# Optimization experiments

Hardware: AMD Instinct MI355X
Metric: run time of the kernel (lower is better)

Reference implementation:

```python
import jax, jax.numpy as jnp
import numpy as np

N_NODES = 100000
N_EDGES = 3200000
N_GRAPHS = 512
IN_CH = 50
HID = 256


def setup_inputs() -> dict:
    key = jax.random.key(0)
    ks = jax.random.split(key, 8)
    x = jax.random.normal(ks[0], (N_NODES, IN_CH), dtype=jnp.float32)
    edge_index = jax.random.randint(ks[1], (2, N_EDGES), 0, N_NODES, dtype=jnp.int64)
    batch = jnp.sort(jax.random.randint(ks[2], (N_NODES,), 0, N_GRAPHS, dtype=jnp.int64))
    # SAGEConv params: lin_l (applied to aggregated neighbors, with bias), lin_r (root, no bias)
    s_in = 1.0 / np.sqrt(IN_CH)
    W_l = jax.random.uniform(ks[3], (HID, IN_CH), jnp.float32, -s_in, s_in)
    b_l = jax.random.uniform(ks[4], (HID,), jnp.float32, -s_in, s_in)
    W_r = jax.random.uniform(ks[5], (HID, IN_CH), jnp.float32, -s_in, s_in)
    s_h = 1.0 / np.sqrt(HID)
    W_c = jax.random.uniform(ks[6], (2, HID), jnp.float32, -s_h, s_h)
    b_c = jax.random.uniform(ks[7], (2,), jnp.float32, -s_h, s_h)
    return {"x": x, "edge_index": edge_index, "batch": batch,
            "W_l": W_l, "b_l": b_l, "W_r": W_r, "W_c": W_c, "b_c": b_c}


def _segment_mean(vals, seg_ids, num_segments):
    s = jax.ops.segment_sum(vals, seg_ids, num_segments=num_segments)
    cnt = jax.ops.segment_sum(jnp.ones((vals.shape[0],), vals.dtype), seg_ids,
                              num_segments=num_segments)
    return s / jnp.maximum(cnt, 1.0)[:, None]


def reference(x, edge_index, batch, W_l, b_l, W_r, W_c, b_c):
    src, dst = edge_index[0], edge_index[1]
    # SAGEConv: mean-aggregate neighbor features at each target node
    agg = _segment_mean(x[src], dst, N_NODES)          # [N, IN_CH]
    h = agg @ W_l.T + b_l + x @ W_r.T                  # [N, HID]
    h = jax.nn.leaky_relu(h, negative_slope=0.01)
    # dropout p=0.3 is identity in eval mode
    pooled = _segment_mean(h, batch, N_GRAPHS)         # [G, HID]
    return pooled @ W_c.T + b_c                        # [G, 2]
```

## Files before the change

### kernel.cpp

```cpp
#include <hip/hip_runtime.h>

#define N_NODES 100000
#define N_EDGES 3200000
#define N_GRAPHS 512
#define IN_CH 50
#define HID 256
#define NB 391
#define NBLK2 391
#define EPB2 8192

typedef unsigned short ushort_t;
using s16x8 = __attribute__((ext_vector_type(8))) short;
using us8   = __attribute__((ext_vector_type(8))) unsigned short;
using us4   = __attribute__((ext_vector_type(4))) unsigned short;
using f32x4 = __attribute__((ext_vector_type(4))) float;
using f32x2 = __attribute__((ext_vector_type(2))) float;

__device__ __forceinline__ float bf2f(ushort_t u) {
    return __uint_as_float(((unsigned int)u) << 16);
}
__device__ __forceinline__ ushort_t f2bf(float f) {
    unsigned int x = __float_as_uint(f);
    unsigned int r = x + 0x7fffu + ((x >> 16) & 1u);
    return (ushort_t)(r >> 16);
}
__device__ __forceinline__ int clampi(int v, int hi) {
    return v < 0 ? 0 : (v >= hi ? hi - 1 : v);
}

__device__ __forceinline__ unsigned char f2e4(float f) {
    unsigned char s = (unsigned char)((__float_as_uint(f) >> 31) << 7);
    float a = fabsf(f);
    if (a >= 0.015625f) {
        if (a > 448.f) a = 448.f;
        unsigned int u = __float_as_uint(a);
        u += 0x7FFFFu + ((u >> 20) & 1u);
        int e8 = (int)(u >> 23) - 127 + 7;
        unsigned int m8 = (u >> 20) & 7u;
        if (e8 > 15) { e8 = 15; m8 = 6; }
        return s | (unsigned char)((e8 << 3) | m8);
    } else {
        int m = (int)rintf(a * 512.f);
        if (m > 7) return s | 0x08;
        return s | (unsigned char)m;
    }
}
__device__ __forceinline__ float e42f(unsigned int c) {
    unsigned int w = ((c & 0x80u) << 24) | ((c & 0x7fu) << 20);
    return __uint_as_float(w) * 0x1p120f;
}

#if __has_builtin(__builtin_amdgcn_cvt_pk_f32_fp8)
#define ACC4(w, m, pb)                                                     \
    do {                                                                   \
        f32x2 p01 = __builtin_amdgcn_cvt_pk_f32_fp8((int)(w), false);      \
        f32x2 p23 = __builtin_amdgcn_cvt_pk_f32_fp8((int)(w), true);       \
        a2[(pb) + 0] = p01 * (m) + a2[(pb) + 0];                           \
        a2[(pb) + 1] = p23 * (m) + a2[(pb) + 1];                           \
    } while (0)
#else
#define ACC4(w, m, pb)                                                     \
    do {                                                                   \
        f32x2 p01, p23;                                                    \
        p01[0] = e42f((w) & 0xffu);        p01[1] = e42f(((w) >> 8) & 0xffu);  \
        p23[0] = e42f(((w) >> 16) & 0xffu); p23[1] = e42f(((w) >> 24) & 0xffu); \
        a2[(pb) + 0] = p01 * (m) + a2[(pb) + 0];                           \
        a2[(pb) + 1] = p23 * (m) + a2[(pb) + 1];                           \
    } while (0)
#endif

constexpr size_t OFF_GACC   = 0;
constexpr size_t ZBYTES     = 8192;
constexpr size_t OFF_AGG    = 561536;
constexpr size_t OFF_X8     = 13361536;
constexpr size_t OFF_EP     = 19761536;
constexpr size_t OFF_WT     = 32573824;
constexpr size_t OFF_BND    = 32639360;
constexpr size_t OFF_LST    = 32641416;

__global__ __launch_bounds__(512) void k_scatter(const int* __restrict__ ei,
                                                 int* __restrict__ ep,
                                                 ushort_t* __restrict__ lst) {
    __shared__ int hist[NB];
    __shared__ int sa[512];
    __shared__ int sorig[512];
    __shared__ int lstart[NB + 1];
    __shared__ int lcur[NB];
    __shared__ unsigned int eph[EPB2];

    const int blk = blockIdx.x, t = threadIdx.x;
    for (int i = t; i < NB; i += 512) hist[i] = 0;
    __syncthreads();
    const int e0 = blk * EPB2;
    int sv[16], dv[16];
#pragma unroll
    for (int j = 0; j < 16; ++j) {
        int e = e0 + j * 512 + t;
        if (e < N_EDGES) {
            sv[j] = clampi(ei[e], N_NODES);
            dv[j] = clampi(ei[N_EDGES + e], N_NODES);
        } else {
            dv[j] = -1;
        }
    }
#pragma unroll
    for (int j = 0; j < 16; ++j)
        if (dv[j] >= 0) atomicAdd(&hist[dv[j] >> 8], 1);
    __syncthreads();
    int v = (t < NB) ? hist[t] : 0;
    sa[t] = v; sorig[t] = v;
    __syncthreads();
    for (int off = 1; off < 512; off <<= 1) {
        int u = (t >= off) ? sa[t - off] : 0;
        __syncthreads();
        sa[t] += u;
        __syncthreads();
    }
    if (t < NB) { lstart[t] = sa[t] - sorig[t]; lcur[t] = sa[t] - sorig[t]; }
    if (t == NB - 1) lstart[NB] = sa[t];
    __syncthreads();
#pragma unroll
    for (int j = 0; j < 16; ++j) {
        if (dv[j] >= 0) {
            int b = dv[j] >> 8;
            int r = atomicAdd(&lcur[b], 1);
            eph[r] = ((unsigned int)sv[j] << 8) | (unsigned int)(dv[j] & 255);
        }
    }
    __syncthreads();
    int mv = lstart[NB];
    for (int i = t; i < mv; i += 512) ep[e0 + i] = (int)eph[i];
    for (int i = t; i <= NB; i += 512) lst[blk * (NB + 1) + i] = (ushort_t)lstart[i];
}

#define PREP_CONV_BLOCKS 6250
#define PREP_BW_BLOCKS 128
#define PREP_BND_BLOCKS 391
__global__ __launch_bounds__(256) void k_prep(const float* __restrict__ x,
                                              unsigned char* __restrict__ x8,
                                              const float* __restrict__ Wl,
                                              const float* __restrict__ Wr,
                                              ushort_t* __restrict__ WT,
                                              const int* __restrict__ batch,
                                              int* __restrict__ bnd) {
    int blk = blockIdx.x;
    if (blk < PREP_CONV_BLOCKS) {
        int idx = blk * 256 + threadIdx.x;
        int n = idx >> 4, c4 = (idx & 15) << 2;
        uchar4 o;
        o.x = (c4 + 0 < IN_CH) ? f2e4(x[n * IN_CH + c4 + 0]) : (unsigned char)0;
        o.y = (c4 + 1 < IN_CH) ? f2e4(x[n * IN_CH + c4 + 1]) : (unsigned char)0;
        o.z = (c4 + 2 < IN_CH) ? f2e4(x[n * IN_CH + c4 + 2]) : (unsigned char)0;
        o.w = (c4 + 3 < IN_CH) ? f2e4(x[n * IN_CH + c4 + 3]) : (unsigned char)0;
        *(uchar4*)(x8 + (size_t)n * 64 + c4) = o;
    } else if (blk < PREP_CONV_BLOCKS + PREP_BW_BLOCKS) {
        int idx = (blk - PREP_CONV_BLOCKS) * 256 + threadIdx.x;
        int j = idx >> 7;
        int k = idx & 127;
        ushort_t val = 0;
        if (k < IN_CH) val = f2bf(Wl[j * IN_CH + k]);
        else if (k >= 64 && k < 64 + IN_CH) val = f2bf(Wr[j * IN_CH + (k - 64)]);
        WT[idx] = val;
    } else {
        int n = (blk - PREP_CONV_BLOCKS - PREP_BW_BLOCKS) * 256 + threadIdx.x;
        if (n >= N_NODES) return;
        int b = clampi(batch[n], N_GRAPHS);
        if (n == 0) {
            for (int g = 0; g <= b; ++g) bnd[g] = 0;
        } else {
            int a = clampi(batch[n - 1], N_GRAPHS);
            for (int g = a + 1; g <= b; ++g) bnd[g] = n;
        }
        if (n == N_NODES - 1) {
            for (int g = b + 1; g <= N_GRAPHS; ++g) bnd[g] = N_NODES;
        }
    }
}

#define CSR_CAP 10240
__global__ __launch_bounds__(512) void k_csrgather(const int* __restrict__ ep,
                                                   const ushort_t* __restrict__ lst,
                                                   const unsigned char* __restrict__ x8,
                                                   ushort_t* __restrict__ agg) {
    __shared__ int sa[512];
    __shared__ int sorig[512];
    __shared__ int rro[NBLK2 + 1];
    __shared__ int lsa[NBLK2];
    __shared__ ushort_t runof[CSR_CAP];
    __shared__ int ldeg[256];
    __shared__ int aa[256];
    __shared__ int lcur[256];
    __shared__ int excl_s[256];
    __shared__ int lds_src[CSR_CAP];

    const int b = blockIdx.x, t = threadIdx.x;

    int lenv = 0;
    if (t < NBLK2) {
        int lsv = (int)lst[t * (NB + 1) + b];
        int le = (int)lst[t * (NB + 1) + b + 1];
        lenv = le - lsv;
        lsa[t] = lsv;
    }
    sa[t] = lenv; sorig[t] = lenv;
    __syncthreads();
    for (int off = 1; off < 512; off <<= 1) {
        int u = (t >= off) ? sa[t - off] : 0;
        __syncthreads();
        sa[t] += u;
        __syncthreads();
    }
    if (t < NBLK2) rro[t] = sa[t] - sorig[t];
    if (t == NBLK2 - 1) rro[NBLK2] = sa[t];
    __syncthreads();
    int m = rro[NBLK2];
    if (m > CSR_CAP) m = CSR_CAP;

    if (t < NBLK2) {
        int o = rro[t];
        int e = o + lenv;
        if (e > CSR_CAP) e = CSR_CAP;
        for (int j = o; j < e; ++j) runof[j] = (ushort_t)t;
    }
    if (t < 256) ldeg[t] = 0;
    __syncthreads();

    int rv[20];
#pragma unroll
    for (int k = 0; k < 20; ++k) {
        int i = t + k * 512;
        if (i < m) {
            int r = (int)runof[i];
            rv[k] = ep[r * EPB2 + lsa[r] + (i - rro[r])];
        }
    }
#pragma unroll
    for (int k = 0; k < 20; ++k) {
        int i = t + k * 512;
        if (i < m) atomicAdd(&ldeg[rv[k] & 255], 1);
    }
    __syncthreads();
    if (t < 256) aa[t] = ldeg[t];
    __syncthreads();
    for (int off = 1; off < 256; off <<= 1) {
        int u = (t >= off && t < 256) ? aa[t - off] : 0;
        __syncthreads();
        if (t < 256) aa[t] += u;
        __syncthreads();
    }
    if (t < 256) {
        int excl = aa[t] - ldeg[t];
        excl_s[t] = excl;
        lcur[t] = excl;
    }
    __syncthreads();
#pragma unroll
    for (int k = 0; k < 20; ++k) {
        int i = t + k * 512;
        if (i < m) {
            int p = rv[k];
            int r = atomicAdd(&lcur[p & 255], 1);
            lds_src[r] = p >> 8;
        }
    }
    __syncthreads();

    const int wv = t >> 6;
    const int lane = t & 63;
    const int r8 = lane >> 3;
    const int c8 = lane & 7;
    const int cb = c8 << 3;
    for (int k = 0; k < 32; ++k) {
        int ln = wv * 32 + k;
        int gid = (b << 8) + ln;
        if (gid >= N_NODES) break;
        int dg = ldeg[ln];
        int st = excl_s[ln];

        f32x2 a2[4] = {};
        const int nit = (dg + 31) >> 5;
        for (int it = 0; it < nit; ++it) {
            int i0 = (it << 5) + r8;
            int i1 = i0 + 8, i2 = i0 + 16, i3 = i0 + 24;
            int s0 = lds_src[st + (i0 < dg ? i0 : 0)];
            int s1 = lds_src[st + (i1 < dg ? i1 : 0)];
            int s2 = lds_src[st + (i2 < dg ? i2 : 0)];
            int s3 = lds_src[st + (i3 < dg ? i3 : 0)];
            uint2 w0 = *(const uint2*)(x8 + (size_t)s0 * 64 + cb);
            uint2 w1 = *(const uint2*)(x8 + (size_t)s1 * 64 + cb);
            uint2 w2 = *(const uint2*)(x8 + (size_t)s2 * 64 + cb);
            uint2 w3 = *(const uint2*)(x8 + (size_t)s3 * 64 + cb);
            float m0 = i0 < dg ? 1.f : 0.f;
            float m1 = i1 < dg ? 1.f : 0.f;
            float m2 = i2 < dg ? 1.f : 0.f;
            float m3 = i3 < dg ? 1.f : 0.f;
            ACC4(w0.x, m0, 0); ACC4(w0.y, m0, 2);
            ACC4(w1.x, m1, 0); ACC4(w1.y, m1, 2);
            ACC4(w2.x, m2, 0); ACC4(w2.y, m2, 2);
            ACC4(w3.x, m3, 0); ACC4(w3.y, m3, 2);
        }
#pragma unroll
        for (int p = 0; p < 4; ++p) {
            a2[p][0] += __shfl_xor(a2[p][0], 8);
            a2[p][1] += __shfl_xor(a2[p][1], 8);
            a2[p][0] += __shfl_xor(a2[p][0], 16);
            a2[p][1] += __shfl_xor(a2[p][1], 16);
            a2[p][0] += __shfl_xor(a2[p][0], 32);
            a2[p][1] += __shfl_xor(a2[p][1], 32);
        }
        float inv = 1.0f / (float)(dg > 1 ? dg : 1);
        if (r8 == 0) {
            us8 o;
#pragma unroll
            for (int q = 0; q < 8; ++q) o[q] = f2bf(a2[q >> 1][q & 1] * inv);
            *(us8*)(agg + (size_t)gid * 64 + cb) = o;
        }
    }
}

__global__ __launch_bounds__(256) void k_convb(const float* __restrict__ x,
                                               ushort_t* __restrict__ xb) {
    int t = blockIdx.x * blockDim.x + threadIdx.x;
    if (t >= N_NODES * 16) return;
    int n = t >> 4, c4 = (t & 15) << 2;
    us4 o;
#pragma unroll
    for (int j = 0; j < 4; j++) {
        int c = c4 + j;
        o[j] = (c < IN_CH) ? f2bf(x[n * IN_CH + c]) : (ushort_t)0;
    }
    *(us4*)(xb + (size_t)n * 64 + c4) = o;
}

__global__ __launch_bounds__(256) void k_gemm(const ushort_t* __restrict__ agg,
                                              const ushort_t* __restrict__ xb,
                                              const ushort_t* __restrict__ WT,
                                              const float* __restrict__ bl,
                                              const float* __restrict__ Wc,
                                              const int* __restrict__ batch,
                                              float* __restrict__ gacc) {
    __shared__ ushort_t Alds[64 * 136];
    __shared__ float ypart[4][64][2];
    __shared__ float gred[64][2];

    const int t = threadIdx.x;
    const int w = t >> 6;
    const int lane = t & 63;
    const int quad = lane >> 4;
    const int r16 = lane & 15;
    const int brow0 = blockIdx.x * 128;

    if (t < 128) gred[t >> 1][t & 1] = 0.f;

    s16x8 bfr[4][4];
#pragma unroll
    for (int s = 0; s < 4; ++s)
#pragma unroll
        for (int ni = 0; ni < 4; ++ni)
            bfr[s][ni] = *(const s16x8*)(WT + (size_t)(w * 64 + 16 * ni + r16) * 128
                                            + s * 32 + (quad << 3));

    float blv[4], w0v[4], w1v[4];
#pragma unroll
    for (int ni = 0; ni < 4; ni++) {
        int col = w * 64 + 16 * ni + r16;
        blv[ni] = bl[col];
        w0v[ni] = Wc[col];
        w1v[ni] = Wc[HID + col];
    }

    int lastb = brow0 + 127;
    if (lastb >= N_NODES) lastb = N_NODES - 1;
    const int gmin = clampi(batch[brow0], N_GRAPHS);
    const int gmax = clampi(batch[lastb], N_GRAPHS);
    const int gspan = gmax - gmin + 1;
    const bool use_lds = (gspan <= 64);

    for (int r4 = 0; r4 < 2; ++r4) {
        const int row0 = brow0 + r4 * 64;
        __syncthreads();
        {
            int row = t >> 2;
            int q4 = t & 3;
            int gr = row0 + row;
            us8* dst = (us8*)&Alds[row * 136 + q4 * 32];
            if (gr < N_NODES) {
                const us8* src = (q4 < 2)
                    ? (const us8*)(agg + (size_t)gr * 64 + (q4 & 1) * 32)
                    : (const us8*)(xb + (size_t)gr * 64 + (q4 & 1) * 32);
                dst[0] = src[0];
                dst[1] = src[1];
                dst[2] = src[2];
                dst[3] = src[3];
            } else {
                us8 z = {0, 0, 0, 0, 0, 0, 0, 0};
                dst[0] = z; dst[1] = z; dst[2] = z; dst[3] = z;
            }
        }
        __syncthreads();

        f32x4 acc[4][4] = {};
#pragma unroll
        for (int s = 0; s < 4; ++s) {
            s16x8 af[4];
#pragma unroll
            for (int mi = 0; mi < 4; mi++)
                af[mi] = *(const s16x8*)&Alds[(16 * mi + r16) * 136 + s * 32 + (quad << 3)];
#pragma unroll
            for (int mi = 0; mi < 4; mi++)
#pragma unroll
                for (int ni = 0; ni < 4; ni++)
                    acc[mi][ni] = __builtin_amdgcn_mfma_f32_16x16x32_bf16(
                        af[mi], bfr[s][ni], acc[mi][ni], 0, 0, 0);
        }

#pragma unroll
        for (int mi = 0; mi < 4; mi++) {
#pragma unroll
            for (int r = 0; r < 4; r++) {
                float p0 = 0.f, p1 = 0.f;
#pragma unroll
                for (int ni = 0; ni < 4; ni++) {
                    float h = acc[mi][ni][r] + blv[ni];
                    h = (h > 0.f) ? h : 0.01f * h;
                    p0 = fmaf(h, w0v[ni], p0);
                    p1 = fmaf(h, w1v[ni], p1);
                }
#pragma unroll
                for (int off = 1; off < 16; off <<= 1) {
                    p0 += __shfl_xor(p0, off, 16);
                    p1 += __shfl_xor(p1, off, 16);
                }
                if (r16 == 0) {
                    int rl = 16 * mi + (quad << 2) + r;
                    ypart[w][rl][0] = p0;
                    ypart[w][rl][1] = p1;
                }
            }
        }
        __syncthreads();

        if (t < 128) {
            int rl = t >> 1, cc = t & 1;
            int node = row0 + rl;
            if (node < N_NODES) {
                float s = ypart[0][rl][cc] + ypart[1][rl][cc]
                        + ypart[2][rl][cc] + ypart[3][rl][cc];
                int g = clampi(batch[node], N_GRAPHS);
                if (use_lds) atomicAdd(&gred[g - gmin][cc], s);
                else atomicAdd(&gacc[g * 2 + cc], s);
            }
        }
    }
    __syncthreads();
    if (use_lds && t < gspan * 2) {
        int gg = t >> 1, c2 = t & 1;
        float v = gred[gg][c2];
        if (v != 0.f) atomicAdd(&gacc[(gmin + gg) * 2 + c2], v);
    }
}

__global__ void k_fin(const float* __restrict__ gacc, const int* __restrict__ bnd,
                      const float* __restrict__ bc, float* __restrict__ out) {
    int t = blockIdx.x * blockDim.x + threadIdx.x;
    if (t < N_GRAPHS * 2) {
        int g = t >> 1, c = t & 1;
        int cnt = bnd[g + 1] - bnd[g];
        out[t] = gacc[t] / (float)(cnt > 1 ? cnt : 1) + bc[c];
    }
}

extern "C" void kernel_launch(void* const* d_in, const int* in_sizes, int n_in,
                              void* d_out, int out_size, void* d_ws, size_t ws_size,
                              hipStream_t stream) {
    const float* x  = (const float*)d_in[0];
    const int* ei   = (const int*)d_in[1];
    const int* batch= (const int*)d_in[2];
    const float* Wl = (const float*)d_in[3];
    const float* bl = (const float*)d_in[4];
    const float* Wr = (const float*)d_in[5];
    const float* Wc = (const float*)d_in[6];
    const float* bc = (const float*)d_in[7];
    float* out = (float*)d_out;

    char* ws = (char*)d_ws;
    float* gacc        = (float*)(ws + OFF_GACC);
    ushort_t* agg      = (ushort_t*)(ws + OFF_AGG);
    unsigned char* x8  = (unsigned char*)(ws + OFF_X8);
    int* ep            = (int*)(ws + OFF_EP);
    ushort_t* xb       = (ushort_t*)(ws + OFF_EP);
    ushort_t* WT       = (ushort_t*)(ws + OFF_WT);
    int* bnd           = (int*)(ws + OFF_BND);
    ushort_t* lst      = (ushort_t*)(ws + OFF_LST);

    hipMemsetAsync(ws, 0, ZBYTES, stream);
    k_scatter    <<<NBLK2, 512, 0, stream>>>(ei, ep, lst);
    k_prep       <<<PREP_CONV_BLOCKS + PREP_BW_BLOCKS + PREP_BND_BLOCKS, 256, 0, stream>>>(
                     x, x8, Wl, Wr, WT, batch, bnd);
    k_csrgather  <<<NB, 512, 0, stream>>>(ep, lst, x8, agg);
    k_convb      <<<(N_NODES * 16 + 255) / 256, 256, 0, stream>>>(x, xb);
    k_gemm       <<<(N_NODES + 127) / 128, 256, 0, stream>>>(agg, xb, WT, bl, Wc, batch, gacc);
    k_fin        <<<4, 256, 0, stream>>>(gacc, bnd, bc, out);
}
```

Baseline: 224.2 us.

## Process two nodes per wave in CSR gather; replace GEMM shuffle reduction with LDS reduce

The CSR gather loop now handles two destination nodes per iteration, issuing eight independent x8 row loads instead of four to raise memory-level parallelism. Both accumulators are then reduced with a shared wave-reduction helper. LDS use is cut by aliasing runof onto lds_src and reusing sa in place of aa. In the GEMM epilogue, the 16-lane shuffle reduction is replaced by writing per-lane partials to a padded LDS array, which 64 threads then sum serially. This trades more LDS traffic and a serial 64-term sum per thread for fewer shuffles.

```diff
diff --git a/kernel.cpp b/kernel.cpp
--- a/kernel.cpp
+++ b/kernel.cpp
@@ -50,24 +50,36 @@
     return __uint_as_float(w) * 0x1p120f;
 }
 
+__device__ __forceinline__ void acc8(f32x2 a2[4], uint2 w, float m) {
 #if __has_builtin(__builtin_amdgcn_cvt_pk_f32_fp8)
-#define ACC4(w, m, pb)                                                     \
-    do {                                                                   \
-        f32x2 p01 = __builtin_amdgcn_cvt_pk_f32_fp8((int)(w), false);      \
-        f32x2 p23 = __builtin_amdgcn_cvt_pk_f32_fp8((int)(w), true);       \
-        a2[(pb) + 0] = p01 * (m) + a2[(pb) + 0];                           \
-        a2[(pb) + 1] = p23 * (m) + a2[(pb) + 1];                           \
-    } while (0)
+    f32x2 p0 = __builtin_amdgcn_cvt_pk_f32_fp8((int)w.x, false);
+    f32x2 p1 = __builtin_amdgcn_cvt_pk_f32_fp8((int)w.x, true);
+    f32x2 p2 = __builtin_amdgcn_cvt_pk_f32_fp8((int)w.y, false);
+    f32x2 p3 = __builtin_amdgcn_cvt_pk_f32_fp8((int)w.y, true);
 #else
-#define ACC4(w, m, pb)                                                     \
-    do {                                                                   \
-        f32x2 p01, p23;                                                    \
-        p01[0] = e42f((w) & 0xffu);        p01[1] = e42f(((w) >> 8) & 0xffu);  \
-        p23[0] = e42f(((w) >> 16) & 0xffu); p23[1] = e42f(((w) >> 24) & 0xffu); \
-        a2[(pb) + 0] = p01 * (m) + a2[(pb) + 0];                           \
-        a2[(pb) + 1] = p23 * (m) + a2[(pb) + 1];                           \
-    } while (0)
+    f32x2 p0, p1, p2, p3;
+    p0[0] = e42f(w.x & 0xffu);         p0[1] = e42f((w.x >> 8) & 0xffu);
+    p1[0] = e42f((w.x >> 16) & 0xffu); p1[1] = e42f((w.x >> 24) & 0xffu);
+    p2[0] = e42f(w.y & 0xffu);         p2[1] = e42f((w.y >> 8) & 0xffu);
+    p3[0] = e42f((w.y >> 16) & 0xffu); p3[1] = e42f((w.y >> 24) & 0xffu);
 #endif
+    a2[0] = p0 * m + a2[0];
+    a2[1] = p1 * m + a2[1];
+    a2[2] = p2 * m + a2[2];
+    a2[3] = p3 * m + a2[3];
+}
+
+__device__ __forceinline__ void wavered(f32x2 a2[4]) {
+#pragma unroll
+    for (int p = 0; p < 4; ++p) {
+        a2[p][0] += __shfl_xor(a2[p][0], 8);
+        a2[p][1] += __shfl_xor(a2[p][1], 8);
+        a2[p][0] += __shfl_xor(a2[p][0], 16);
+        a2[p][1] += __shfl_xor(a2[p][1], 16);
+        a2[p][0] += __shfl_xor(a2[p][0], 32);
+        a2[p][1] += __shfl_xor(a2[p][1], 32);
+    }
+}
 
 constexpr size_t OFF_GACC   = 0;
 constexpr size_t ZBYTES     = 8192;
@@ -186,12 +198,11 @@
     __shared__ int sorig[512];
     __shared__ int rro[NBLK2 + 1];
     __shared__ int lsa[NBLK2];
-    __shared__ ushort_t runof[CSR_CAP];
     __shared__ int ldeg[256];
-    __shared__ int aa[256];
     __shared__ int lcur[256];
     __shared__ int excl_s[256];
     __shared__ int lds_src[CSR_CAP];
+    ushort_t* runof = (ushort_t*)lds_src;
 
     const int b = blockIdx.x, t = threadIdx.x;
 
@@ -240,16 +251,16 @@
         if (i < m) atomicAdd(&ldeg[rv[k] & 255], 1);
     }
     __syncthreads();
-    if (t < 256) aa[t] = ldeg[t];
+    if (t < 256) sa[t] = ldeg[t];
     __syncthreads();
     for (int off = 1; off < 256; off <<= 1) {
-        int u = (t >= off && t < 256) ? aa[t - off] : 0;
-        __syncthreads();
-        if (t < 256) aa[t] += u;
+        int u = (t >= off && t < 256) ? sa[t - off] : 0;
+        __syncthreads();
+        if (t < 256) sa[t] += u;
         __syncthreads();
     }
     if (t < 256) {
-        int excl = aa[t] - ldeg[t];
+        int excl = sa[t] - ldeg[t];
         excl_s[t] = excl;
         lcur[t] = excl;
     }
@@ -270,50 +281,62 @@
     const int r8 = lane >> 3;
     const int c8 = lane & 7;
     const int cb = c8 << 3;
-    for (int k = 0; k < 32; ++k) {
-        int ln = wv * 32 + k;
-        int gid = (b << 8) + ln;
-        if (gid >= N_NODES) break;
-        int dg = ldeg[ln];
-        int st = excl_s[ln];
+    for (int k = 0; k < 32; k += 2) {
+        int ln0 = wv * 32 + k;
+        int gid0 = (b << 8) + ln0;
+        if (gid0 >= N_NODES) break;
+        int ok1 = (gid0 + 1 < N_NODES) ? 1 : 0;
+        int dg0 = ldeg[ln0], st0 = excl_s[ln0];
+        int dg1 = ok1 ? ldeg[ln0 + 1] : 0;
+        int st1 = ok1 ? excl_s[ln0 + 1] : st0;
 
         f32x2 a2[4] = {};
-        const int nit = (dg + 31) >> 5;
+        f32x2 c2[4] = {};
+        int dgm = dg0 > dg1 ? dg0 : dg1;
+        int nit = (dgm + 31) >> 5;
         for (int it = 0; it < nit; ++it) {
             int i0 = (it << 5) + r8;
             int i1 = i0 + 8, i2 = i0 + 16, i3 = i0 + 24;
-            int s0 = lds_src[st + (i0 < dg ? i0 : 0)];
-            int s1 = lds_src[st + (i1 < dg ? i1 : 0)];
-            int s2 = lds_src[st + (i2 < dg ? i2 : 0)];
-            int s3 = lds_src[st + (i3 < dg ? i3 : 0)];
-            uint2 w0 = *(const uint2*)(x8 + (size_t)s0 * 64 + cb);
-            uint2 w1 = *(const uint2*)(x8 + (size_t)s1 * 64 + cb);
-            uint2 w2 = *(const uint2*)(x8 + (size_t)s2 * 64 + cb);
-            uint2 w3 = *(const uint2*)(x8 + (size_t)s3 * 64 + cb);
-            float m0 = i0 < dg ? 1.f : 0.f;
-            float m1 = i1 < dg ? 1.f : 0.f;
-            float m2 = i2 < dg ? 1.f : 0.f;
-            float m3 = i3 < dg ? 1.f : 0.f;
-            ACC4(w0.x, m0, 0); ACC4(w0.y, m0, 2);
-            ACC4(w1.x, m1, 0); ACC4(w1.y, m1, 2);
-            ACC4(w2.x, m2, 0); ACC4(w2.y, m2, 2);
-            ACC4(w3.x, m3, 0); ACC4(w3.y, m3, 2);
-        }
-#pragma unroll
-        for (int p = 0; p < 4; ++p) {
-            a2[p][0] += __shfl_xor(a2[p][0], 8);
-            a2[p][1] += __shfl_xor(a2[p][1], 8);
-            a2[p][0] += __shfl_xor(a2[p][0], 16);
-            a2[p][1] += __shfl_xor(a2[p][1], 16);
-            a2[p][0] += __shfl_xor(a2[p][0], 32);
-            a2[p][1] += __shfl_xor(a2[p][1], 32);
-        }
-        float inv = 1.0f / (float)(dg > 1 ? dg : 1);
+            int sA = lds_src[st0 + (i0 < dg0 ? i0 : 0)];
+            int sB = lds_src[st0 + (i1 < dg0 ? i1 : 0)];
+            int sC = lds_src[st0 + (i2 < dg0 ? i2 : 0)];
+            int sD = lds_src[st0 + (i3 < dg0 ? i3 : 0)];
+            int sE = lds_src[st1 + (i0 < dg1 ? i0 : 0)];
+            int sF = lds_src[st1 + (i1 < dg1 ? i1 : 0)];
+            int sG = lds_src[st1 + (i2 < dg1 ? i2 : 0)];
+            int sH = lds_src[st1 + (i3 < dg1 ? i3 : 0)];
+            uint2 wA = *(const uint2*)(x8 + (size_t)sA * 64 + cb);
+            uint2 wB = *(const uint2*)(x8 + (size_t)sB * 64 + cb);
+            uint2 wC = *(const uint2*)(x8 + (size_t)sC * 64 + cb);
+            uint2 wD = *(const uint2*)(x8 + (size_t)sD * 64 + cb);
+            uint2 wE = *(const uint2*)(x8 + (size_t)sE * 64 + cb);
+            uint2 wF = *(const uint2*)(x8 + (size_t)sF * 64 + cb);
+            uint2 wG = *(const uint2*)(x8 + (size_t)sG * 64 + cb);
+            uint2 wH = *(const uint2*)(x8 + (size_t)sH * 64 + cb);
+            acc8(a2, wA, i0 < dg0 ? 1.f : 0.f);
+            acc8(a2, wB, i1 < dg0 ? 1.f : 0.f);
+            acc8(a2, wC, i2 < dg0 ? 1.f : 0.f);
+            acc8(a2, wD, i3 < dg0 ? 1.f : 0.f);
+            acc8(c2, wE, i0 < dg1 ? 1.f : 0.f);
+            acc8(c2, wF, i1 < dg1 ? 1.f : 0.f);
+            acc8(c2, wG, i2 < dg1 ? 1.f : 0.f);
+            acc8(c2, wH, i3 < dg1 ? 1.f : 0.f);
+        }
+        wavered(a2);
+        wavered(c2);
         if (r8 == 0) {
+            float inv0 = 1.0f / (float)(dg0 > 1 ? dg0 : 1);
             us8 o;
 #pragma unroll
-            for (int q = 0; q < 8; ++q) o[q] = f2bf(a2[q >> 1][q & 1] * inv);
-            *(us8*)(agg + (size_t)gid * 64 + cb) = o;
+            for (int q = 0; q < 8; ++q) o[q] = f2bf(a2[q >> 1][q & 1] * inv0);
+            *(us8*)(agg + (size_t)gid0 * 64 + cb) = o;
+            if (ok1) {
+                float inv1 = 1.0f / (float)(dg1 > 1 ? dg1 : 1);
+                us8 o1;
+#pragma unroll
+                for (int q = 0; q < 8; ++q) o1[q] = f2bf(c2[q >> 1][q & 1] * inv1);
+                *(us8*)(agg + (size_t)(gid0 + 1) * 64 + cb) = o1;
+            }
         }
     }
 }
@@ -340,7 +363,7 @@
                                               const int* __restrict__ batch,
                                               float* __restrict__ gacc) {
     __shared__ ushort_t Alds[64 * 136];
-    __shared__ float ypart[4][64][2];
+    __shared__ f32x2 yp[4][64][17];
     __shared__ float gred[64][2];
 
     const int t = threadIdx.x;
@@ -426,29 +449,30 @@
                     p0 = fmaf(h, w0v[ni], p0);
                     p1 = fmaf(h, w1v[ni], p1);
                 }
-#pragma unroll
-                for (int off = 1; off < 16; off <<= 1) {
-                    p0 += __shfl_xor(p0, off, 16);
-                    p1 += __shfl_xor(p1, off, 16);
+                int rl = 16 * mi + (quad << 2) + r;
+                f32x2 pv; pv[0] = p0; pv[1] = p1;
+                yp[w][rl][r16] = pv;
+            }
+        }
+        __syncthreads();
+
+        if (t < 64) {
+            f32x2 s; s[0] = 0.f; s[1] = 0.f;
+#pragma unroll
+            for (int ww = 0; ww < 4; ++ww)
+#pragma unroll
+                for (int j = 0; j < 16; ++j)
+                    s = s + yp[ww][t][j];
+            int node = row0 + t;
+            if (node < N_NODES) {
+                int g = clampi(batch[node], N_GRAPHS);
+                if (use_lds) {
+                    atomicAdd(&gred[g - gmin][0], s[0]);
+                    atomicAdd(&gred[g - gmin][1], s[1]);
+                } else {
+                    atomicAdd(&gacc[g * 2 + 0], s[0]);
+                    atomicAdd(&gacc[g * 2 + 1], s[1]);
                 }
-                if (r16 == 0) {
-                    int rl = 16 * mi + (quad << 2) + r;
-                    ypart[w][rl][0] = p0;
-                    ypart[w][rl][1] = p1;
-                }
-            }
-        }
-        __syncthreads();
-
-        if (t < 128) {
-            int rl = t >> 1, cc = t & 1;
-            int node = row0 + rl;
-            if (node < N_NODES) {
-                float s = ypart[0][rl][cc] + ypart[1][rl][cc]
-                        + ypart[2][rl][cc] + ypart[3][rl][cc];
-                int g = clampi(batch[node], N_GRAPHS);
-                if (use_lds) atomicAdd(&gred[g - gmin][cc], s);
-                else atomicAdd(&gacc[g * 2 + cc], s);
             }
         }
     }
```

New measurement: 209.3 us. 1.07x faster.
